# Kernel optimization log

Measured on AMD Instinct MI355X. Metric: run time of the kernel, lower is better.

## Reference

```python
import jax, jax.numpy as jnp
import numpy as np

B, N = 4, 65536
NUM_GROUP, GROUP_SIZE = 512, 64
EMB = 60


def setup_inputs() -> dict:
    key = jax.random.key(0)
    ks = jax.random.split(key, 8)
    inp = {
        'xyz': jax.random.uniform(ks[0], (B, N, 3), jnp.float32),
        'color': jax.random.uniform(ks[1], (B, N, 3), jnp.float32),
        'W1': jax.random.normal(ks[2], (6, 64), jnp.float32) * 0.2,
        'b1': jnp.zeros((64,), jnp.float32),
        'W2': jax.random.normal(ks[3], (64, 128), jnp.float32) * 0.1,
        'b2': jnp.zeros((128,), jnp.float32),
        'W3': jax.random.normal(ks[4], (128, 256), jnp.float32) * 0.08,
        'b3': jnp.zeros((256,), jnp.float32),
        'W4': jax.random.normal(ks[5], (256, 512), jnp.float32) * 0.06,
        'b4': jnp.zeros((512,), jnp.float32),
        'Wp': jax.random.normal(ks[6], (512, EMB), jnp.float32) * 0.04,
        'bp': jnp.zeros((EMB,), jnp.float32),
    }
    return inp


def fps(xyz, n):
    """Farthest point sampling. xyz: (B,N,3) -> centers (B,n,3)."""
    b, npts, _ = xyz.shape
    start = jnp.zeros((b,), jnp.int32)
    d0 = jnp.full((b, npts), 1e10, xyz.dtype)

    def step(carry, _):
        dists, last = carry
        p = jnp.take_along_axis(xyz, last[:, None, None], axis=1)  # (B,1,3)
        d = jnp.sum((xyz - p) ** 2, axis=-1)                       # (B,N)
        dists = jnp.minimum(dists, d)
        nxt = jnp.argmax(dists, axis=-1).astype(jnp.int32)
        return (dists, nxt), nxt

    (_, _), rest = jax.lax.scan(step, (d0, start), None, length=n - 1)
    idx = jnp.concatenate([start[:, None], rest.T], axis=1)        # (B,n)
    return jax.vmap(lambda pts, i: pts[i])(xyz, idx)


def knn_idx(k, xyz, new_xyz):
    """Indices of k nearest points in xyz for each query in new_xyz.
    xyz: (B,N,3), new_xyz: (B,S,3) -> (B,S,k) int32. Matches
    square_distance + topk(largest=False)."""
    sq = (jnp.sum(new_xyz ** 2, -1)[..., None]
          + jnp.sum(xyz ** 2, -1)[:, None, :]
          - 2.0 * jnp.einsum('bsc,bnc->bsn', new_xyz, xyz))        # (B,S,N)
    _, idx = jax.lax.top_k(-sq, k)
    return idx


def reference(xyz, color, W1, b1, W2, b2, W3, b3, W4, b4, Wp, bp):
    # --- Group: FPS centers + KNN neighborhood gather + centering ---
    center = fps(xyz, NUM_GROUP)                                   # (B,G,3)
    idx = knn_idx(GROUP_SIZE, xyz, center)                         # (B,G,M)
    gather = jax.vmap(lambda pts, i: pts[i])                       # pts[(B,)N,3], i (G,M)
    neighborhood = gather(xyz, idx) - center[:, :, None, :]        # (B,G,M,3) centered
    neighborhood_color = gather(color, idx)                        # (B,G,M,3)
    feats = jnp.concatenate([neighborhood, neighborhood_color], -1)  # (B,G,M,6)

    # --- PointNet: per-point MLP -> max over group -> projection ---
    x = jax.nn.relu(feats @ W1 + b1)
    x = jax.nn.relu(x @ W2 + b2)
    x = jax.nn.relu(x @ W3 + b3)
    x = jax.nn.relu(x @ W4 + b4)                                   # (B,G,M,512)
    x = jnp.max(x, axis=2)                                         # (B,G,512)
    emb = x @ Wp + bp                                              # (B,G,60)
    return emb, center
```

## Files before the change

kernel.cpp:

```cpp
#include <hip/hip_runtime.h>
#include <stdint.h>

#define DI __device__ __forceinline__

typedef _Float16 f16x8 __attribute__((ext_vector_type(8)));
typedef float f32x4 __attribute__((ext_vector_type(4)));

constexpr int kB = 4;
constexpr int kN = 65536;
constexpr int kG = 512;
constexpr int kM = 64;
constexpr int kE = 60;
constexpr int GRD = 20;
constexpr int NCELL = GRD * GRD * GRD;
constexpr float CW = 1.0f / 20.0f;

constexpr int FPS_SUB = 8;
constexpr int FPS_PT_T = kN / FPS_SUB / 1024;

constexpr size_t OFF_WIN    = 0;
constexpr size_t OFF_CCNT   = OFF_WIN + (size_t)kB * kG * 256;
constexpr size_t ZERO_BYTES = OFF_CCNT + (size_t)kB * NCELL * 4;
constexpr size_t OFF_CSTART = ZERO_BYTES;
constexpr size_t OFF_CUR    = OFF_CSTART + (size_t)kB * (NCELL + 1) * 4;
constexpr size_t OFF_SW1    = ((OFF_CUR + (size_t)kB * NCELL * 4) + 255) & ~(size_t)255;
constexpr size_t OFF_SW2    = OFF_SW1 + 2048 * 2;
constexpr size_t OFF_SW3    = OFF_SW2 + 8192 * 2;
constexpr size_t OFF_SW4    = OFF_SW3 + 32768 * 2;
constexpr size_t OFF_WPT    = OFF_SW4 + 131072 * 2;
constexpr size_t OFF_SORT   = ((OFF_WPT + 60 * 512 * 4) + 255) & ~(size_t)255;
constexpr size_t OFF_KIDX   = OFF_SORT + (size_t)kB * kN * 16;

DI int cellof(float x) {
  int c = (int)(x * (float)GRD);
  return min(GRD - 1, max(0, c));
}
DI unsigned orderable(float f) {
  unsigned u = __float_as_uint(f);
  return (u & 0x80000000u) ? ~u : (u | 0x80000000u);
}

__global__ void k_zero(uint32_t* p, int nwords) {
  int i = blockIdx.x * blockDim.x + threadIdx.x;
  int st = gridDim.x * blockDim.x;
  for (; i < nwords; i += st) p[i] = 0u;
}

DI void swz(const float* __restrict__ W, _Float16* __restrict__ sw,
            int total, int nks, int Kreal, int N, int i0, int st) {
  for (int i = i0; i < total; i += st) {
    int j = i & 7, lane = (i >> 3) & 63, rest = i >> 9;
    int ks = rest % nks, nt = rest / nks;
    int k = ks * 32 + ((lane >> 4) << 3) + j;
    int n = nt * 16 + (lane & 15);
    sw[i] = (_Float16)((k < Kreal) ? W[k * N + n] : 0.f);
  }
}

__global__ void k_prep(const float* __restrict__ W1, const float* __restrict__ W2,
                       const float* __restrict__ W3, const float* __restrict__ W4,
                       const float* __restrict__ Wp,
                       _Float16* __restrict__ sw1, _Float16* __restrict__ sw2,
                       _Float16* __restrict__ sw3, _Float16* __restrict__ sw4,
                       float* __restrict__ wpt) {
  int i0 = blockIdx.x * blockDim.x + threadIdx.x;
  int st = gridDim.x * blockDim.x;
  swz(W1, sw1, 2048, 1, 6, 64, i0, st);
  swz(W2, sw2, 8192, 2, 64, 128, i0, st);
  swz(W3, sw3, 32768, 4, 128, 256, i0, st);
  swz(W4, sw4, 131072, 8, 256, 512, i0, st);
  for (int i = i0; i < 60 * 512; i += st) { int n = i >> 9, k = i & 511; wpt[i] = Wp[k * 60 + n]; }
}

DI void redstep(unsigned long long& k, float& x, float& y, float& z, int off) {
  unsigned long long ok = __shfl_down(k, off);
  float ox = __shfl_down(x, off);
  float oy = __shfl_down(y, off);
  float oz = __shfl_down(z, off);
  if (ok > k) { k = ok; x = ox; y = oy; z = oz; }
}

__global__ __launch_bounds__(1024) void k_fps(const float* __restrict__ xyz,
                                              float* __restrict__ outC,
                                              unsigned long long* __restrict__ win) {
  const int b = blockIdx.x >> 3, sub = blockIdx.x & 7;
  const int tid = threadIdx.x;
  const int wave = tid >> 6, lane = tid & 63;
  const float* X = xyz + (size_t)b * kN * 3;
  float px[FPS_PT_T], py[FPS_PT_T], pz[FPS_PT_T], dd[FPS_PT_T];
#pragma unroll
  for (int j = 0; j < FPS_PT_T; ++j) {
    int p = sub * (kN / FPS_SUB) + j * 1024 + tid;
    px[j] = X[3 * p]; py[j] = X[3 * p + 1]; pz[j] = X[3 * p + 2];
    dd[j] = 1e10f;
  }
  float lx = X[0], ly = X[1], lz = X[2];
  if (sub == 0 && tid == 0) {
    outC[(size_t)b * kG * 3 + 0] = lx;
    outC[(size_t)b * kG * 3 + 1] = ly;
    outC[(size_t)b * kG * 3 + 2] = lz;
  }
  __shared__ unsigned long long wkey[16];
  __shared__ float wx[16], wy[16], wz[16];
  __shared__ float sp[3];
  unsigned long long* winB = win + (size_t)b * kG * 32;

  for (int it = 1; it < kG; ++it) {
    unsigned long long bk = 0ull;
    float bx = 0.f, by = 0.f, bz = 0.f;
#pragma unroll
    for (int j = 0; j < FPS_PT_T; ++j) {
      float dx = __fsub_rn(px[j], lx);
      float dy = __fsub_rn(py[j], ly);
      float dz = __fsub_rn(pz[j], lz);
      float d = __fadd_rn(__fadd_rn(__fmul_rn(dx, dx), __fmul_rn(dy, dy)), __fmul_rn(dz, dz));
      float nd = fminf(dd[j], d);
      dd[j] = nd;
      int p = sub * (kN / FPS_SUB) + j * 1024 + tid;
      unsigned long long pk = (1ull << 63) | ((unsigned long long)__float_as_uint(nd) << 16) |
                              (unsigned long long)(0xFFFFu - (unsigned)p);
      if (pk > bk) { bk = pk; bx = px[j]; by = py[j]; bz = pz[j]; }
    }
#pragma unroll
    for (int off = 32; off; off >>= 1) redstep(bk, bx, by, bz, off);
    if (lane == 0) { wkey[wave] = bk; wx[wave] = bx; wy[wave] = by; wz[wave] = bz; }
    __syncthreads();
    if (wave == 0) {
      unsigned long long k2 = (lane < 16) ? wkey[lane] : 0ull;
      float x2 = (lane < 16) ? wx[lane] : 0.f;
      float y2 = (lane < 16) ? wy[lane] : 0.f;
      float z2 = (lane < 16) ? wz[lane] : 0.f;
      redstep(k2, x2, y2, z2, 8);
      redstep(k2, x2, y2, z2, 4);
      redstep(k2, x2, y2, z2, 2);
      redstep(k2, x2, y2, z2, 1);
      unsigned long long* base = winB + (size_t)it * 32;
      if (lane == 0) {
        unsigned long long xyv = ((unsigned long long)__float_as_uint(x2) << 32) |
                                 (unsigned long long)__float_as_uint(y2);
        __hip_atomic_store(base + 8 + sub, xyv, __ATOMIC_RELAXED, __HIP_MEMORY_SCOPE_AGENT);
        __hip_atomic_store(base + 16 + sub, (unsigned long long)__float_as_uint(z2),
                           __ATOMIC_RELAXED, __HIP_MEMORY_SCOPE_AGENT);
        __hip_atomic_store(base + sub, k2, __ATOMIC_RELEASE, __HIP_MEMORY_SCOPE_AGENT);
      }
      int s = lane & 7;
      unsigned long long kk;
      long bail = 0;
      for (;;) {
        kk = __hip_atomic_load(base + s, __ATOMIC_ACQUIRE, __HIP_MEMORY_SCOPE_AGENT);
        unsigned long long rdy = __ballot(kk >> 63);
        if (rdy == ~0ull) break;
        if (++bail > 100000000L) break;
      }
      unsigned long long xyv = __hip_atomic_load(base + 8 + s, __ATOMIC_RELAXED,
                                                 __HIP_MEMORY_SCOPE_AGENT);
      unsigned long long zv = __hip_atomic_load(base + 16 + s, __ATOMIC_RELAXED,
                                                __HIP_MEMORY_SCOPE_AGENT);
      float fx = __uint_as_float((unsigned)(xyv >> 32));
      float fy = __uint_as_float((unsigned)(xyv & 0xFFFFFFFFu));
      float fz = __uint_as_float((unsigned)(zv & 0xFFFFFFFFu));
      redstep(kk, fx, fy, fz, 4);
      redstep(kk, fx, fy, fz, 2);
      redstep(kk, fx, fy, fz, 1);
      if (lane == 0) {
        sp[0] = fx; sp[1] = fy; sp[2] = fz;
        if (sub == 0) {
          outC[((size_t)b * kG + it) * 3 + 0] = fx;
          outC[((size_t)b * kG + it) * 3 + 1] = fy;
          outC[((size_t)b * kG + it) * 3 + 2] = fz;
        }
      }
    }
    __syncthreads();
    lx = sp[0]; ly = sp[1]; lz = sp[2];
  }
}

__global__ void k_cellcount(const float* __restrict__ xyz, uint32_t* __restrict__ ccnt) {
  int i = blockIdx.x * blockDim.x + threadIdx.x;
  int st = gridDim.x * blockDim.x;
  for (; i < kB * kN; i += st) {
    int b = i >> 16, p = i & (kN - 1);
    const float* q = xyz + ((size_t)b * kN + p) * 3;
    int cid = (cellof(q[2]) * GRD + cellof(q[1])) * GRD + cellof(q[0]);
    atomicAdd(&ccnt[b * NCELL + cid], 1u);
  }
}

__global__ void k_scan(const uint32_t* __restrict__ ccnt, uint32_t* __restrict__ cstart,
                       uint32_t* __restrict__ cur) {
  int b = blockIdx.x, tid = threadIdx.x;
  const uint32_t* cc = ccnt + (size_t)b * NCELL;
  uint32_t* cs = cstart + (size_t)b * (NCELL + 1);
  uint32_t* cu = cur + (size_t)b * NCELL;
  __shared__ uint32_t part[256];
  const int chunk = 32;
  int c0 = tid * chunk;
  uint32_t s = 0;
  for (int i = 0; i < chunk; ++i) { int c = c0 + i; if (c < NCELL) s += cc[c]; }
  part[tid] = s;
  __syncthreads();
  for (int off = 1; off < 256; off <<= 1) {
    uint32_t add = (tid >= off) ? part[tid - off] : 0u;
    __syncthreads();
    part[tid] += add;
    __syncthreads();
  }
  uint32_t run = part[tid] - s;
  for (int i = 0; i < chunk; ++i) {
    int c = c0 + i;
    if (c < NCELL) { cs[c] = run; cu[c] = run; run += cc[c]; }
  }
  if (tid == 255) cs[NCELL] = run;
}

__global__ void k_scatter(const float* __restrict__ xyz, uint32_t* __restrict__ cur,
                          float4* __restrict__ sorted) {
  int i = blockIdx.x * blockDim.x + threadIdx.x;
  int st = gridDim.x * blockDim.x;
  for (; i < kB * kN; i += st) {
    int b = i >> 16, p = i & (kN - 1);
    const float* q = xyz + ((size_t)b * kN + p) * 3;
    float x = q[0], y = q[1], z = q[2];
    int cid = (cellof(z) * GRD + cellof(y)) * GRD + cellof(x);
    uint32_t pos = atomicAdd(&cur[b * NCELL + cid], 1u);
    sorted[(size_t)b * kN + pos] = make_float4(x, y, z, __uint_as_float((unsigned)p));
  }
}

constexpr int CAP = 8192;

DI void bitonic(unsigned long long* a, int n, int tid) {
  for (int k = 2; k <= n; k <<= 1)
    for (int j = k >> 1; j > 0; j >>= 1) {
      __syncthreads();
      for (int i = tid; i < n; i += 256) {
        int ix = i ^ j;
        if (ix > i) {
          unsigned long long x = a[i], y = a[ix];
          bool up = ((i & k) == 0);
          if ((x > y) == up) { a[i] = y; a[ix] = x; }
        }
      }
    }
  __syncthreads();
}

__global__ __launch_bounds__(256) void k_knn(const float4* __restrict__ sorted,
                                             const uint32_t* __restrict__ cstart,
                                             const float* __restrict__ outC,
                                             uint32_t* __restrict__ kidx) {
  const int bi = blockIdx.x;
  const int b = (bi & 7) >> 1;
  const int g = ((bi >> 3) << 1) | (bi & 1);
  const int tid = threadIdx.x;
  __shared__ unsigned long long cand[CAP];
  __shared__ int nC;
  const float cx = outC[((size_t)b * kG + g) * 3 + 0];
  const float cy = outC[((size_t)b * kG + g) * 3 + 1];
  const float cz = outC[((size_t)b * kG + g) * 3 + 2];
  const float nc = __fadd_rn(__fadd_rn(__fmul_rn(cx, cx), __fmul_rn(cy, cy)), __fmul_rn(cz, cz));
  const float4* SP = sorted + (size_t)b * kN;
  const uint32_t* CS = cstart + (size_t)b * (NCELL + 1);
  const int ccx = cellof(cx), ccy = cellof(cy), ccz = cellof(cz);
  if (tid == 0) nC = 0;
  __syncthreads();
  int plox = 1, phix = 0, ploy = 1, phiy = 0, ploz = 1, phiz = 0;
  for (int r = 1; r <= GRD; ++r) {
    int lox = max(0, ccx - r), hix = min(GRD - 1, ccx + r);
    int loy = max(0, ccy - r), hiy = min(GRD - 1, ccy + r);
    int loz = max(0, ccz - r), hiz = min(GRD - 1, ccz + r);
    for (int z = loz; z <= hiz; ++z)
      for (int y = loy; y <= hiy; ++y) {
        bool rowPrev = (r > 1) && (z >= ploz && z <= phiz && y >= ploy && y <= phiy);
        for (int s = 0; s < 2; ++s) {
          int xa, xb;
          if (!rowPrev) { if (s) break; xa = lox; xb = hix; }
          else if (s == 0) { xa = lox; xb = plox - 1; }
          else { xa = phix + 1; xb = hix; }
          if (xa > xb) continue;
          int c0 = (z * GRD + y) * GRD + xa;
          int i0 = CS[c0];
          int i1 = CS[(z * GRD + y) * GRD + xb + 1];
          for (int i = i0 + tid; i < i1; i += 256) {
            float4 pt = SP[i];
            float npn = __fadd_rn(__fadd_rn(__fmul_rn(pt.x, pt.x), __fmul_rn(pt.y, pt.y)),
                                  __fmul_rn(pt.z, pt.z));
            float dot = __fadd_rn(__fadd_rn(__fmul_rn(cx, pt.x), __fmul_rn(cy, pt.y)),
                                  __fmul_rn(cz, pt.z));
            float sq = __fsub_rn(__fadd_rn(nc, npn), __fmul_rn(2.0f, dot));
            unsigned key = orderable(sq);
            int pos = atomicAdd(&nC, 1);
            if (pos < CAP)
              cand[pos] = ((unsigned long long)key << 32) | (unsigned)__float_as_uint(pt.w);
          }
        }
      }
    __syncthreads();
    int n = min(nC, CAP);
    float rc = 1e30f;
    if (lox > 0) rc = fminf(rc, cx - (float)lox * CW);
    if (hix < GRD - 1) rc = fminf(rc, (float)(hix + 1) * CW - cx);
    if (loy > 0) rc = fminf(rc, cy - (float)loy * CW);
    if (hiy < GRD - 1) rc = fminf(rc, (float)(hiy + 1) * CW - cy);
    if (loz > 0) rc = fminf(rc, cz - (float)loz * CW);
    if (hiz < GRD - 1) rc = fminf(rc, (float)(hiz + 1) * CW - cz);
    float r2 = (rc >= 1e29f) ? 3.0e38f : rc * rc * (1.0f - 1e-5f);
    unsigned keyR = orderable(r2);
    bool done = false;
    if (n >= kM) {
      int np2 = 1;
      while (np2 < n) np2 <<= 1;
      for (int i = n + tid; i < np2; i += 256) cand[i] = ~0ull;
      bitonic(cand, np2, tid);
      unsigned k63 = (unsigned)(cand[kM - 1] >> 32);
      done = (k63 <= keyR);
      if (tid == 0) nC = n;
    }
    __syncthreads();
    if (done) break;
    plox = lox; phix = hix; ploy = loy; phiy = hiy; ploz = loz; phiz = hiz;
  }
  if (tid < kM)
    kidx[((size_t)b * kG + g) * kM + tid] = (uint32_t)(cand[tid] & 0xFFFFFFFFu);
}

template <int Kdim, int Ndim, int SIN, int SOUT>
DI void mfma_layer(const _Float16* __restrict__ Xin, _Float16* __restrict__ Xout,
                   const _Float16* __restrict__ Wsw, const float* __restrict__ bias,
                   int wave, int lane) {
  constexpr int NKS = Kdim / 32;
  constexpr int NTW = Ndim / 64;
  constexpr int CH = (NTW < 4) ? NTW : 4;
  const int quad = lane >> 4, l16 = lane & 15;
  for (int c0 = 0; c0 < NTW; c0 += CH) {
    f32x4 acc[CH][4];
#pragma unroll
    for (int nt = 0; nt < CH; ++nt) {
      float bv = bias[wave * (Ndim / 4) + (c0 + nt) * 16 + l16];
#pragma unroll
      for (int m = 0; m < 4; ++m) acc[nt][m] = {bv, bv, bv, bv};
    }
#pragma unroll
    for (int ks = 0; ks < NKS; ++ks) {
      f16x8 af[4];
#pragma unroll
      for (int m = 0; m < 4; ++m)
        af[m] = *(const f16x8*)(Xin + (m * 16 + l16) * SIN + ks * 32 + quad * 8);
#pragma unroll
      for (int nt = 0; nt < CH; ++nt) {
        int ntg = wave * NTW + c0 + nt;
        f16x8 bf = *(const f16x8*)(Wsw + ((size_t)(ntg * NKS + ks) * 64 + lane) * 8);
#pragma unroll
        for (int m = 0; m < 4; ++m)
          acc[nt][m] = __builtin_amdgcn_mfma_f32_16x16x32_f16(af[m], bf, acc[nt][m], 0, 0, 0);
      }
    }
#pragma unroll
    for (int nt = 0; nt < CH; ++nt) {
      int col = wave * (Ndim / 4) + (c0 + nt) * 16 + l16;
#pragma unroll
      for (int m = 0; m < 4; ++m)
#pragma unroll
        for (int r = 0; r < 4; ++r) {
          int row = m * 16 + quad * 4 + r;
          Xout[row * SOUT + col] = (_Float16)fmaxf(acc[nt][m][r], 0.f);
        }
    }
  }
}

DI void mfma_layer4(const _Float16* __restrict__ Xin, const _Float16* __restrict__ Wsw,
                    const float* __restrict__ bias, float* __restrict__ maxv,
                    int wave, int lane) {
  constexpr int SIN = 264, NKS = 8, NTW = 8, CH = 4;
  const int quad = lane >> 4, l16 = lane & 15;
  for (int c0 = 0; c0 < NTW; c0 += CH) {
    f32x4 acc[CH][4];
#pragma unroll
    for (int nt = 0; nt < CH; ++nt) {
      float bv = bias[wave * 128 + (c0 + nt) * 16 + l16];
#pragma unroll
      for (int m = 0; m < 4; ++m) acc[nt][m] = {bv, bv, bv, bv};
    }
#pragma unroll
    for (int ks = 0; ks < NKS; ++ks) {
      f16x8 af[4];
#pragma unroll
      for (int m = 0; m < 4; ++m)
        af[m] = *(const f16x8*)(Xin + (m * 16 + l16) * SIN + ks * 32 + quad * 8);
#pragma unroll
      for (int nt = 0; nt < CH; ++nt) {
        int ntg = wave * NTW + c0 + nt;
        f16x8 bf = *(const f16x8*)(Wsw + ((size_t)(ntg * NKS + ks) * 64 + lane) * 8);
#pragma unroll
        for (int m = 0; m < 4; ++m)
          acc[nt][m] = __builtin_amdgcn_mfma_f32_16x16x32_f16(af[m], bf, acc[nt][m], 0, 0, 0);
      }
    }
#pragma unroll
    for (int nt = 0; nt < CH; ++nt) {
      float mx = 0.f;
#pragma unroll
      for (int m = 0; m < 4; ++m)
#pragma unroll
        for (int r = 0; r < 4; ++r) mx = fmaxf(mx, acc[nt][m][r]);
      mx = fmaxf(mx, __shfl_xor(mx, 16, 64));
      mx = fmaxf(mx, __shfl_xor(mx, 32, 64));
      if (quad == 0) maxv[wave * 128 + (c0 + nt) * 16 + l16] = mx;
    }
  }
}

__global__ __launch_bounds__(256) void k_mlp(
    const float* __restrict__ xyz, const float* __restrict__ color,
    const float* __restrict__ outC, const uint32_t* __restrict__ kidx,
    const _Float16* __restrict__ sw1, const _Float16* __restrict__ sw2,
    const _Float16* __restrict__ sw3, const _Float16* __restrict__ sw4,
    const float* __restrict__ wpt,
    const float* __restrict__ b1, const float* __restrict__ b2,
    const float* __restrict__ b3, const float* __restrict__ b4,
    const float* __restrict__ bp, float* __restrict__ outE) {
  const int bi = blockIdx.x;
  const int b = (bi & 7) >> 1;
  const int g = ((bi >> 3) << 1) | (bi & 1);
  const int tid = threadIdx.x;
  const int wave = tid >> 6, lane = tid & 63;
  __shared__ __align__(16) char smem[17408 + 33792];
  _Float16* bufA = (_Float16*)smem;
  _Float16* bufB = (_Float16*)(smem + 17408);
  float* maxv = (float*)smem;
  float* psum = (float*)(smem + 2048);

  if (tid < kM) {
    uint32_t p = kidx[((size_t)b * kG + g) * kM + tid];
    const float* cen = outC + ((size_t)b * kG + g) * 3;
    const float* xp = xyz + ((size_t)b * kN + p) * 3;
    const float* cp = color + ((size_t)b * kN + p) * 3;
    f16x8 v = {};
    v[0] = (_Float16)__fsub_rn(xp[0], cen[0]);
    v[1] = (_Float16)__fsub_rn(xp[1], cen[1]);
    v[2] = (_Float16)__fsub_rn(xp[2], cen[2]);
    v[3] = (_Float16)cp[0];
    v[4] = (_Float16)cp[1];
    v[5] = (_Float16)cp[2];
    f16x8 z = {};
    *(f16x8*)(bufA + tid * 40 + 0) = v;
    *(f16x8*)(bufA + tid * 40 + 8) = z;
    *(f16x8*)(bufA + tid * 40 + 16) = z;
    *(f16x8*)(bufA + tid * 40 + 24) = z;
  }
  __syncthreads();
  mfma_layer<32, 64, 40, 72>(bufA, bufB, sw1, b1, wave, lane);
  __syncthreads();
  mfma_layer<64, 128, 72, 136>(bufB, bufA, sw2, b2, wave, lane);
  __syncthreads();
  mfma_layer<128, 256, 136, 264>(bufA, bufB, sw3, b3, wave, lane);
  __syncthreads();
  mfma_layer4(bufB, sw4, b4, maxv, wave, lane);
  __syncthreads();
  if (tid < 240) {
    int j = tid >> 2, q = tid & 3;
    const float* w = wpt + (size_t)j * 512 + q * 128;
    float s = 0.f;
#pragma unroll 4
    for (int k = 0; k < 128; ++k) s = fmaf(maxv[q * 128 + k], w[k], s);
    psum[tid] = s;
  }
  __syncthreads();
  if (tid < kE) {
    float e = __fadd_rn(__fadd_rn(psum[tid * 4 + 0], psum[tid * 4 + 1]),
                        __fadd_rn(psum[tid * 4 + 2], psum[tid * 4 + 3])) + bp[tid];
    outE[((size_t)b * kG + g) * kE + tid] = e;
  }
}

extern "C" void kernel_launch(void* const* d_in, const int* in_sizes, int n_in,
                              void* d_out, int out_size, void* d_ws, size_t ws_size,
                              hipStream_t stream) {
  (void)in_sizes; (void)n_in; (void)out_size; (void)ws_size;
  const float* xyz = (const float*)d_in[0];
  const float* color = (const float*)d_in[1];
  const float* W1 = (const float*)d_in[2];
  const float* b1 = (const float*)d_in[3];
  const float* W2 = (const float*)d_in[4];
  const float* b2 = (const float*)d_in[5];
  const float* W3 = (const float*)d_in[6];
  const float* b3 = (const float*)d_in[7];
  const float* W4 = (const float*)d_in[8];
  const float* b4 = (const float*)d_in[9];
  const float* Wp = (const float*)d_in[10];
  const float* bp = (const float*)d_in[11];

  char* ws = (char*)d_ws;
  auto win = (unsigned long long*)(ws + OFF_WIN);
  auto ccnt = (uint32_t*)(ws + OFF_CCNT);
  auto cstart = (uint32_t*)(ws + OFF_CSTART);
  auto cur = (uint32_t*)(ws + OFF_CUR);
  auto sw1 = (_Float16*)(ws + OFF_SW1);
  auto sw2 = (_Float16*)(ws + OFF_SW2);
  auto sw3 = (_Float16*)(ws + OFF_SW3);
  auto sw4 = (_Float16*)(ws + OFF_SW4);
  auto wpt = (float*)(ws + OFF_WPT);
  auto sorted = (float4*)(ws + OFF_SORT);
  auto kidx = (uint32_t*)(ws + OFF_KIDX);

  float* outE = (float*)d_out;
  float* outC = outE + (size_t)kB * kG * kE;

  k_zero<<<128, 256, 0, stream>>>((uint32_t*)ws, (int)(ZERO_BYTES / 4));
  k_prep<<<256, 256, 0, stream>>>(W1, W2, W3, W4, Wp, sw1, sw2, sw3, sw4, wpt);
  k_fps<<<kB * FPS_SUB, 1024, 0, stream>>>(xyz, outC, win);
  k_cellcount<<<512, 256, 0, stream>>>(xyz, ccnt);
  k_scan<<<kB, 256, 0, stream>>>(ccnt, cstart, cur);
  k_scatter<<<512, 256, 0, stream>>>(xyz, cur, sorted);
  k_knn<<<kB * kG, 256, 0, stream>>>(sorted, cstart, outC, kidx);
  k_mlp<<<kB * kG, 256, 0, stream>>>(xyz, color, outC, kidx, sw1, sw2, sw3, sw4, wpt,
                                     b1, b2, b3, b4, bp, outE);
}
```

Measured before the change: 2.379 ms.

## Restructure FPS cross-block exchange into leader-gather and broadcast with per-block cache lines

The per-iteration exchange among the 8 FPS sub-blocks changes from all-to-all polling to a leader scheme. Sub-blocks 1-7 each write their candidate to their own 64-byte line. Sub-block 0 gathers those seven, reduces them with its own result, and publishes the winner to one broadcast line that the others poll, with s_sleep inside the spin loops. The aim is to cut contention from many blocks polling shared cache lines and to reduce false sharing. The cost is an extra serial hop (gather, then broadcast) on the critical path of every iteration, and a workspace window twice as large to zero.

```diff
diff --git a/kernel.cpp b/kernel.cpp
--- a/kernel.cpp
+++ b/kernel.cpp
@@ -19,7 +19,7 @@
 constexpr int FPS_PT_T = kN / FPS_SUB / 1024;
 
 constexpr size_t OFF_WIN    = 0;
-constexpr size_t OFF_CCNT   = OFF_WIN + (size_t)kB * kG * 256;
+constexpr size_t OFF_CCNT   = OFF_WIN + (size_t)kB * kG * 512;
 constexpr size_t ZERO_BYTES = OFF_CCNT + (size_t)kB * NCELL * 4;
 constexpr size_t OFF_CSTART = ZERO_BYTES;
 constexpr size_t OFF_CUR    = OFF_CSTART + (size_t)kB * (NCELL + 1) * 4;
@@ -102,8 +102,10 @@
   }
   __shared__ unsigned long long wkey[16];
   __shared__ float wx[16], wy[16], wz[16];
+  __shared__ unsigned long long selfk;
+  __shared__ float selfx, selfy, selfz;
   __shared__ float sp[3];
-  unsigned long long* winB = win + (size_t)b * kG * 32;
+  unsigned long long* winB = win + (size_t)b * kG * 64;
 
   for (int it = 1; it < kG; ++it) {
     unsigned long long bk = 0ull;
@@ -134,40 +136,74 @@
       redstep(k2, x2, y2, z2, 4);
       redstep(k2, x2, y2, z2, 2);
       redstep(k2, x2, y2, z2, 1);
-      unsigned long long* base = winB + (size_t)it * 32;
-      if (lane == 0) {
-        unsigned long long xyv = ((unsigned long long)__float_as_uint(x2) << 32) |
-                                 (unsigned long long)__float_as_uint(y2);
-        __hip_atomic_store(base + 8 + sub, xyv, __ATOMIC_RELAXED, __HIP_MEMORY_SCOPE_AGENT);
-        __hip_atomic_store(base + 16 + sub, (unsigned long long)__float_as_uint(z2),
-                           __ATOMIC_RELAXED, __HIP_MEMORY_SCOPE_AGENT);
-        __hip_atomic_store(base + sub, k2, __ATOMIC_RELEASE, __HIP_MEMORY_SCOPE_AGENT);
-      }
-      int s = lane & 7;
-      unsigned long long kk;
-      long bail = 0;
-      for (;;) {
-        kk = __hip_atomic_load(base + s, __ATOMIC_ACQUIRE, __HIP_MEMORY_SCOPE_AGENT);
-        unsigned long long rdy = __ballot(kk >> 63);
-        if (rdy == ~0ull) break;
-        if (++bail > 100000000L) break;
-      }
-      unsigned long long xyv = __hip_atomic_load(base + 8 + s, __ATOMIC_RELAXED,
-                                                 __HIP_MEMORY_SCOPE_AGENT);
-      unsigned long long zv = __hip_atomic_load(base + 16 + s, __ATOMIC_RELAXED,
-                                                __HIP_MEMORY_SCOPE_AGENT);
-      float fx = __uint_as_float((unsigned)(xyv >> 32));
-      float fy = __uint_as_float((unsigned)(xyv & 0xFFFFFFFFu));
-      float fz = __uint_as_float((unsigned)(zv & 0xFFFFFFFFu));
-      redstep(kk, fx, fy, fz, 4);
-      redstep(kk, fx, fy, fz, 2);
-      redstep(kk, fx, fy, fz, 1);
-      if (lane == 0) {
-        sp[0] = fx; sp[1] = fy; sp[2] = fz;
-        if (sub == 0) {
+      unsigned long long* base = winB + (size_t)it * 64;
+      unsigned long long* bc = base + 56;
+      if (sub == 0) {
+        if (lane == 0) { selfk = k2; selfx = x2; selfy = y2; selfz = z2; }
+        unsigned long long* line = base + (size_t)((lane < 7) ? lane : 0) * 8;
+        unsigned long long kk = 0ull;
+        long bail = 0;
+        for (;;) {
+          if (lane < 7)
+            kk = __hip_atomic_load(line, __ATOMIC_ACQUIRE, __HIP_MEMORY_SCOPE_AGENT);
+          bool rdy = (lane >= 7) || ((kk >> 63) & 1ull);
+          if (__ballot(rdy) == ~0ull) break;
+          __builtin_amdgcn_s_sleep(1);
+          if (++bail > 100000000L) break;
+        }
+        float fx = 0.f, fy = 0.f, fz = 0.f;
+        if (lane < 7) {
+          unsigned long long xyv = __hip_atomic_load(line + 1, __ATOMIC_RELAXED,
+                                                     __HIP_MEMORY_SCOPE_AGENT);
+          unsigned long long zv = __hip_atomic_load(line + 2, __ATOMIC_RELAXED,
+                                                    __HIP_MEMORY_SCOPE_AGENT);
+          fx = __uint_as_float((unsigned)(xyv >> 32));
+          fy = __uint_as_float((unsigned)(xyv & 0xFFFFFFFFu));
+          fz = __uint_as_float((unsigned)(zv & 0xFFFFFFFFu));
+        } else if (lane == 7) {
+          kk = selfk; fx = selfx; fy = selfy; fz = selfz;
+        } else {
+          kk = 0ull;
+        }
+        redstep(kk, fx, fy, fz, 4);
+        redstep(kk, fx, fy, fz, 2);
+        redstep(kk, fx, fy, fz, 1);
+        if (lane == 0) {
+          unsigned long long xyv = ((unsigned long long)__float_as_uint(fx) << 32) |
+                                   (unsigned long long)__float_as_uint(fy);
+          __hip_atomic_store(bc + 1, xyv, __ATOMIC_RELAXED, __HIP_MEMORY_SCOPE_AGENT);
+          __hip_atomic_store(bc + 2, (unsigned long long)__float_as_uint(fz),
+                             __ATOMIC_RELAXED, __HIP_MEMORY_SCOPE_AGENT);
+          __hip_atomic_store(bc, kk, __ATOMIC_RELEASE, __HIP_MEMORY_SCOPE_AGENT);
+          sp[0] = fx; sp[1] = fy; sp[2] = fz;
           outC[((size_t)b * kG + it) * 3 + 0] = fx;
           outC[((size_t)b * kG + it) * 3 + 1] = fy;
           outC[((size_t)b * kG + it) * 3 + 2] = fz;
+        }
+      } else {
+        if (lane == 0) {
+          unsigned long long* line = base + (size_t)(sub - 1) * 8;
+          unsigned long long xyv = ((unsigned long long)__float_as_uint(x2) << 32) |
+                                   (unsigned long long)__float_as_uint(y2);
+          __hip_atomic_store(line + 1, xyv, __ATOMIC_RELAXED, __HIP_MEMORY_SCOPE_AGENT);
+          __hip_atomic_store(line + 2, (unsigned long long)__float_as_uint(z2),
+                             __ATOMIC_RELAXED, __HIP_MEMORY_SCOPE_AGENT);
+          __hip_atomic_store(line, k2, __ATOMIC_RELEASE, __HIP_MEMORY_SCOPE_AGENT);
+          unsigned long long kk;
+          long bail = 0;
+          for (;;) {
+            kk = __hip_atomic_load(bc, __ATOMIC_ACQUIRE, __HIP_MEMORY_SCOPE_AGENT);
+            if (kk >> 63) break;
+            __builtin_amdgcn_s_sleep(1);
+            if (++bail > 100000000L) break;
+          }
+          unsigned long long xy2 = __hip_atomic_load(bc + 1, __ATOMIC_RELAXED,
+                                                     __HIP_MEMORY_SCOPE_AGENT);
+          unsigned long long zv2 = __hip_atomic_load(bc + 2, __ATOMIC_RELAXED,
+                                                     __HIP_MEMORY_SCOPE_AGENT);
+          sp[0] = __uint_as_float((unsigned)(xy2 >> 32));
+          sp[1] = __uint_as_float((unsigned)(xy2 & 0xFFFFFFFFu));
+          sp[2] = __uint_as_float((unsigned)(zv2 & 0xFFFFFFFFu));
         }
       }
     }
@@ -508,7 +544,7 @@
   float* outE = (float*)d_out;
   float* outC = outE + (size_t)kB * kG * kE;
 
-  k_zero<<<128, 256, 0, stream>>>((uint32_t*)ws, (int)(ZERO_BYTES / 4));
+  k_zero<<<160, 256, 0, stream>>>((uint32_t*)ws, (int)(ZERO_BYTES / 4));
   k_prep<<<256, 256, 0, stream>>>(W1, W2, W3, W4, Wp, sw1, sw2, sw3, sw4, wpt);
   k_fps<<<kB * FPS_SUB, 1024, 0, stream>>>(xyz, outC, win);
   k_cellcount<<<512, 256, 0, stream>>>(xyz, ccnt);
```

New measurement: 2.912 ms. 22.4% more time.

## Run FPS on cell-sorted points with per-segment bounding-box pruning in one block

Applied to the files above, without the earlier changes.

FPS now runs after the spatial cell sort, using one 1024-thread block per batch. Each thread owns a contiguous segment of 64 spatially sorted points and keeps their min-distances in registers, plus the segment's bounding box. When the box's lower-bound distance to the new center cannot reduce the segment's current maximum, the thread skips the distance update. This removes the cross-block atomic spin synchronization of the 8-block version at the cost of using only 4 CUs. Ties are broken by original index carried in the sorted w field, though the key layout differs, and the 64-entry register array may spill.

```diff
diff --git a/kernel.cpp b/kernel.cpp
--- a/kernel.cpp
+++ b/kernel.cpp
@@ -15,11 +15,9 @@
 constexpr int NCELL = GRD * GRD * GRD;
 constexpr float CW = 1.0f / 20.0f;
 
-constexpr int FPS_SUB = 8;
-constexpr int FPS_PT_T = kN / FPS_SUB / 1024;
-
-constexpr size_t OFF_WIN    = 0;
-constexpr size_t OFF_CCNT   = OFF_WIN + (size_t)kB * kG * 256;
+constexpr int SEG = 64;
+
+constexpr size_t OFF_CCNT   = 0;
 constexpr size_t ZERO_BYTES = OFF_CCNT + (size_t)kB * NCELL * 4;
 constexpr size_t OFF_CSTART = ZERO_BYTES;
 constexpr size_t OFF_CUR    = OFF_CSTART + (size_t)kB * (NCELL + 1) * 4;
@@ -72,110 +70,6 @@
   for (int i = i0; i < 60 * 512; i += st) { int n = i >> 9, k = i & 511; wpt[i] = Wp[k * 60 + n]; }
 }
 
-DI void redstep(unsigned long long& k, float& x, float& y, float& z, int off) {
-  unsigned long long ok = __shfl_down(k, off);
-  float ox = __shfl_down(x, off);
-  float oy = __shfl_down(y, off);
-  float oz = __shfl_down(z, off);
-  if (ok > k) { k = ok; x = ox; y = oy; z = oz; }
-}
-
-__global__ __launch_bounds__(1024) void k_fps(const float* __restrict__ xyz,
-                                              float* __restrict__ outC,
-                                              unsigned long long* __restrict__ win) {
-  const int b = blockIdx.x >> 3, sub = blockIdx.x & 7;
-  const int tid = threadIdx.x;
-  const int wave = tid >> 6, lane = tid & 63;
-  const float* X = xyz + (size_t)b * kN * 3;
-  float px[FPS_PT_T], py[FPS_PT_T], pz[FPS_PT_T], dd[FPS_PT_T];
-#pragma unroll
-  for (int j = 0; j < FPS_PT_T; ++j) {
-    int p = sub * (kN / FPS_SUB) + j * 1024 + tid;
-    px[j] = X[3 * p]; py[j] = X[3 * p + 1]; pz[j] = X[3 * p + 2];
-    dd[j] = 1e10f;
-  }
-  float lx = X[0], ly = X[1], lz = X[2];
-  if (sub == 0 && tid == 0) {
-    outC[(size_t)b * kG * 3 + 0] = lx;
-    outC[(size_t)b * kG * 3 + 1] = ly;
-    outC[(size_t)b * kG * 3 + 2] = lz;
-  }
-  __shared__ unsigned long long wkey[16];
-  __shared__ float wx[16], wy[16], wz[16];
-  __shared__ float sp[3];
-  unsigned long long* winB = win + (size_t)b * kG * 32;
-
-  for (int it = 1; it < kG; ++it) {
-    unsigned long long bk = 0ull;
-    float bx = 0.f, by = 0.f, bz = 0.f;
-#pragma unroll
-    for (int j = 0; j < FPS_PT_T; ++j) {
-      float dx = __fsub_rn(px[j], lx);
-      float dy = __fsub_rn(py[j], ly);
-      float dz = __fsub_rn(pz[j], lz);
-      float d = __fadd_rn(__fadd_rn(__fmul_rn(dx, dx), __fmul_rn(dy, dy)), __fmul_rn(dz, dz));
-      float nd = fminf(dd[j], d);
-      dd[j] = nd;
-      int p = sub * (kN / FPS_SUB) + j * 1024 + tid;
-      unsigned long long pk = (1ull << 63) | ((unsigned long long)__float_as_uint(nd) << 16) |
-                              (unsigned long long)(0xFFFFu - (unsigned)p);
-      if (pk > bk) { bk = pk; bx = px[j]; by = py[j]; bz = pz[j]; }
-    }
-#pragma unroll
-    for (int off = 32; off; off >>= 1) redstep(bk, bx, by, bz, off);
-    if (lane == 0) { wkey[wave] = bk; wx[wave] = bx; wy[wave] = by; wz[wave] = bz; }
-    __syncthreads();
-    if (wave == 0) {
-      unsigned long long k2 = (lane < 16) ? wkey[lane] : 0ull;
-      float x2 = (lane < 16) ? wx[lane] : 0.f;
-      float y2 = (lane < 16) ? wy[lane] : 0.f;
-      float z2 = (lane < 16) ? wz[lane] : 0.f;
-      redstep(k2, x2, y2, z2, 8);
-      redstep(k2, x2, y2, z2, 4);
-      redstep(k2, x2, y2, z2, 2);
-      redstep(k2, x2, y2, z2, 1);
-      unsigned long long* base = winB + (size_t)it * 32;
-      if (lane == 0) {
-        unsigned long long xyv = ((unsigned long long)__float_as_uint(x2) << 32) |
-                                 (unsigned long long)__float_as_uint(y2);
-        __hip_atomic_store(base + 8 + sub, xyv, __ATOMIC_RELAXED, __HIP_MEMORY_SCOPE_AGENT);
-        __hip_atomic_store(base + 16 + sub, (unsigned long long)__float_as_uint(z2),
-                           __ATOMIC_RELAXED, __HIP_MEMORY_SCOPE_AGENT);
-        __hip_atomic_store(base + sub, k2, __ATOMIC_RELEASE, __HIP_MEMORY_SCOPE_AGENT);
-      }
-      int s = lane & 7;
-      unsigned long long kk;
-      long bail = 0;
-      for (;;) {
-        kk = __hip_atomic_load(base + s, __ATOMIC_ACQUIRE, __HIP_MEMORY_SCOPE_AGENT);
-        unsigned long long rdy = __ballot(kk >> 63);
-        if (rdy == ~0ull) break;
-        if (++bail > 100000000L) break;
-      }
-      unsigned long long xyv = __hip_atomic_load(base + 8 + s, __ATOMIC_RELAXED,
-                                                 __HIP_MEMORY_SCOPE_AGENT);
-      unsigned long long zv = __hip_atomic_load(base + 16 + s, __ATOMIC_RELAXED,
-                                                __HIP_MEMORY_SCOPE_AGENT);
-      float fx = __uint_as_float((unsigned)(xyv >> 32));
-      float fy = __uint_as_float((unsigned)(xyv & 0xFFFFFFFFu));
-      float fz = __uint_as_float((unsigned)(zv & 0xFFFFFFFFu));
-      redstep(kk, fx, fy, fz, 4);
-      redstep(kk, fx, fy, fz, 2);
-      redstep(kk, fx, fy, fz, 1);
-      if (lane == 0) {
-        sp[0] = fx; sp[1] = fy; sp[2] = fz;
-        if (sub == 0) {
-          outC[((size_t)b * kG + it) * 3 + 0] = fx;
-          outC[((size_t)b * kG + it) * 3 + 1] = fy;
-          outC[((size_t)b * kG + it) * 3 + 2] = fz;
-        }
-      }
-    }
-    __syncthreads();
-    lx = sp[0]; ly = sp[1]; lz = sp[2];
-  }
-}
-
 __global__ void k_cellcount(const float* __restrict__ xyz, uint32_t* __restrict__ ccnt) {
   int i = blockIdx.x * blockDim.x + threadIdx.x;
   int st = gridDim.x * blockDim.x;
@@ -225,6 +119,110 @@
     int cid = (cellof(z) * GRD + cellof(y)) * GRD + cellof(x);
     uint32_t pos = atomicAdd(&cur[b * NCELL + cid], 1u);
     sorted[(size_t)b * kN + pos] = make_float4(x, y, z, __uint_as_float((unsigned)p));
+  }
+}
+
+DI void redstep(unsigned long long& k, float& x, float& y, float& z, int off) {
+  unsigned long long ok = __shfl_down(k, off);
+  float ox = __shfl_down(x, off);
+  float oy = __shfl_down(y, off);
+  float oz = __shfl_down(z, off);
+  if (ok > k) { k = ok; x = ox; y = oy; z = oz; }
+}
+
+DI unsigned long long fpskey(float d, float w) {
+  return ((unsigned long long)__float_as_uint(d) << 32) |
+         (unsigned long long)(0xFFFFFFFFu - __float_as_uint(w));
+}
+
+__global__ __launch_bounds__(1024) void k_fps(const float4* __restrict__ sorted,
+                                              const float* __restrict__ xyz,
+                                              float* __restrict__ outC) {
+  const int b = blockIdx.x;
+  const int tid = threadIdx.x;
+  const int wave = tid >> 6, lane = tid & 63;
+  const float4* SP = sorted + (size_t)b * kN + (size_t)tid * SEG;
+
+  float cx = xyz[(size_t)b * kN * 3 + 0];
+  float cy = xyz[(size_t)b * kN * 3 + 1];
+  float cz = xyz[(size_t)b * kN * 3 + 2];
+  if (tid == 0) {
+    outC[(size_t)b * kG * 3 + 0] = cx;
+    outC[(size_t)b * kG * 3 + 1] = cy;
+    outC[(size_t)b * kG * 3 + 2] = cz;
+  }
+
+  float dd[SEG];
+  float xlo = 1e30f, xhi = -1e30f, ylo = 1e30f, yhi = -1e30f, zlo = 1e30f, zhi = -1e30f;
+  unsigned long long segk = 0ull;
+  float sx = 0.f, sy = 0.f, sz = 0.f;
+#pragma unroll
+  for (int j = 0; j < SEG; ++j) {
+    float4 pt = SP[j];
+    xlo = fminf(xlo, pt.x); xhi = fmaxf(xhi, pt.x);
+    ylo = fminf(ylo, pt.y); yhi = fmaxf(yhi, pt.y);
+    zlo = fminf(zlo, pt.z); zhi = fmaxf(zhi, pt.z);
+    float dx = __fsub_rn(pt.x, cx);
+    float dy = __fsub_rn(pt.y, cy);
+    float dz = __fsub_rn(pt.z, cz);
+    float d = __fadd_rn(__fadd_rn(__fmul_rn(dx, dx), __fmul_rn(dy, dy)), __fmul_rn(dz, dz));
+    dd[j] = d;
+    unsigned long long k = fpskey(d, pt.w);
+    if (k > segk) { segk = k; sx = pt.x; sy = pt.y; sz = pt.z; }
+  }
+
+  __shared__ unsigned long long wk[16];
+  __shared__ float wxs[16], wys[16], wzs[16];
+  __shared__ float bc[3];
+
+  for (int it = 1; it < kG; ++it) {
+    unsigned long long k = segk;
+    float x = sx, y = sy, z = sz;
+#pragma unroll
+    for (int off = 32; off; off >>= 1) redstep(k, x, y, z, off);
+    if (lane == 0) { wk[wave] = k; wxs[wave] = x; wys[wave] = y; wzs[wave] = z; }
+    __syncthreads();
+    if (wave == 0) {
+      unsigned long long k2 = (lane < 16) ? wk[lane] : 0ull;
+      float x2 = (lane < 16) ? wxs[lane] : 0.f;
+      float y2 = (lane < 16) ? wys[lane] : 0.f;
+      float z2 = (lane < 16) ? wzs[lane] : 0.f;
+      redstep(k2, x2, y2, z2, 8);
+      redstep(k2, x2, y2, z2, 4);
+      redstep(k2, x2, y2, z2, 2);
+      redstep(k2, x2, y2, z2, 1);
+      if (lane == 0) {
+        bc[0] = x2; bc[1] = y2; bc[2] = z2;
+        outC[((size_t)b * kG + it) * 3 + 0] = x2;
+        outC[((size_t)b * kG + it) * 3 + 1] = y2;
+        outC[((size_t)b * kG + it) * 3 + 2] = z2;
+      }
+    }
+    __syncthreads();
+    float ncx = bc[0], ncy = bc[1], ncz = bc[2];
+
+    float ax = fmaxf(fmaxf(xlo - ncx, ncx - xhi), 0.f);
+    float ay = fmaxf(fmaxf(ylo - ncy, ncy - yhi), 0.f);
+    float az = fmaxf(fmaxf(zlo - ncz, ncz - zhi), 0.f);
+    float lb2 = ax * ax + ay * ay + az * az;
+    float segmax = __uint_as_float((unsigned)(segk >> 32));
+    if (lb2 * (1.0f - 1e-5f) < segmax) {
+      unsigned long long nk = 0ull;
+      float nx = 0.f, ny = 0.f, nz = 0.f;
+#pragma unroll
+      for (int j = 0; j < SEG; ++j) {
+        float4 pt = SP[j];
+        float dx = __fsub_rn(pt.x, ncx);
+        float dy = __fsub_rn(pt.y, ncy);
+        float dz = __fsub_rn(pt.z, ncz);
+        float d = __fadd_rn(__fadd_rn(__fmul_rn(dx, dx), __fmul_rn(dy, dy)), __fmul_rn(dz, dz));
+        float nd = fminf(dd[j], d);
+        dd[j] = nd;
+        unsigned long long kk = fpskey(nd, pt.w);
+        if (kk > nk) { nk = kk; nx = pt.x; ny = pt.y; nz = pt.z; }
+      }
+      segk = nk; sx = nx; sy = ny; sz = nz;
+    }
   }
 }
 
@@ -493,7 +491,6 @@
   const float* bp = (const float*)d_in[11];
 
   char* ws = (char*)d_ws;
-  auto win = (unsigned long long*)(ws + OFF_WIN);
   auto ccnt = (uint32_t*)(ws + OFF_CCNT);
   auto cstart = (uint32_t*)(ws + OFF_CSTART);
   auto cur = (uint32_t*)(ws + OFF_CUR);
@@ -510,10 +507,10 @@
 
   k_zero<<<128, 256, 0, stream>>>((uint32_t*)ws, (int)(ZERO_BYTES / 4));
   k_prep<<<256, 256, 0, stream>>>(W1, W2, W3, W4, Wp, sw1, sw2, sw3, sw4, wpt);
-  k_fps<<<kB * FPS_SUB, 1024, 0, stream>>>(xyz, outC, win);
   k_cellcount<<<512, 256, 0, stream>>>(xyz, ccnt);
   k_scan<<<kB, 256, 0, stream>>>(ccnt, cstart, cur);
   k_scatter<<<512, 256, 0, stream>>>(xyz, cur, sorted);
+  k_fps<<<kB, 1024, 0, stream>>>(sorted, xyz, outC);
   k_knn<<<kB * kG, 256, 0, stream>>>(sorted, cstart, outC, kidx);
   k_mlp<<<kB * kG, 256, 0, stream>>>(xyz, color, outC, kidx, sw1, sw2, sw3, sw4, wpt,
                                      b1, b2, b3, b4, bp, outE);
```

Result: slower. 5.864 ms (+146.5%).
